# Kernel optimization log

Measured on AMD Instinct MI355X. Metric: run time of the kernel, lower is better.

The kernel has to match this reference:

```python
import jax, jax.numpy as jnp
import numpy as np

HEADS, DIM_HEAD, WINDOW, QK_SCALE = 8, 64, 512, 8.0

def layer_norm(x, g, b, eps=1e-5):
    m = jnp.mean(x, axis=-1, keepdims=True)
    v = jnp.mean(jnp.square(x - m), axis=-1, keepdims=True)
    return (x - m) * jax.lax.rsqrt(v + eps) * g + b

def l2norm(x, eps=1e-12):
    n = jnp.linalg.norm(x, axis=-1, keepdims=True)
    return x / jnp.maximum(n, eps)

def rotate_half(x):
    x1, x2 = jnp.split(x, 2, axis=-1)
    return jnp.concatenate([-x2, x1], axis=-1)

def rotary_xpos(n, dim, scale_base):
    # SinusoidalEmbeddings with use_xpos=True, scale_base = window_size // 2
    inv_freq = 1.0 / (10000.0 ** (jnp.arange(0, dim, 2, dtype=jnp.float32) / dim))
    t = jnp.arange(n, dtype=jnp.float32)
    freqs = t[:, None] * inv_freq[None, :]
    freqs = jnp.concatenate([freqs, freqs], axis=-1)  # (n, dim)
    scale_vec = (jnp.arange(0, dim, 2, dtype=jnp.float32) + 0.4 * dim) / (1.4 * dim)
    power = (t - n // 2) / scale_base
    scale = scale_vec[None, :] ** power[:, None]
    scale = jnp.concatenate([scale, scale], axis=-1)  # (n, dim)
    return freqs, scale

def local_attention(q, k, v):
    # q, k, v: (BH, N, D); causal sliding-window attention, look_backward=1, exact windowsize
    BH, N, D = q.shape
    WS = WINDOW
    W = N // WS
    freqs, xscale = rotary_xpos(N, D, WS // 2)
    cos, sin = jnp.cos(freqs), jnp.sin(freqs)
    q = q * cos * xscale + rotate_half(q) * sin * xscale
    k = k * cos / xscale + rotate_half(k) * sin / xscale

    bq = q.reshape(BH, W, WS, D)
    bk = k.reshape(BH, W, WS, D)
    bv = v.reshape(BH, W, WS, D)

    def look_around(x):  # prepend previous window along key axis -> (BH, W, 2*WS, D)
        padded = jnp.pad(x, ((0, 0), (1, 0), (0, 0), (0, 0)))
        return jnp.concatenate([padded[:, :-1], padded[:, 1:]], axis=2)

    bk2, bv2 = look_around(bk), look_around(bv)

    seq = jnp.arange(N)
    bq_t = seq.reshape(W, WS)
    kpos = jnp.pad(seq.reshape(W, WS), ((1, 0), (0, 0)), constant_values=-1)
    bq_k = jnp.concatenate([kpos[:-1], kpos[1:]], axis=1)  # (W, 2*WS)
    i, j = bq_t[:, :, None], bq_k[:, None, :]
    # causal | exact-windowsize | padding
    mask = (i < j) | (i > j + WS) | (j == -1)

    sim = jnp.einsum('bwid,bwjd->bwij', bq, bk2) * QK_SCALE
    sim = jnp.where(mask[None], -jnp.finfo(sim.dtype).max, sim)
    attn = jax.nn.softmax(sim, axis=-1)
    out = jnp.einsum('bwij,bwjd->bwid', attn, bv2)
    return out.reshape(BH, N, D)

def reference(x, attn_ln_g, attn_ln_b, Wqkv, q_scale, k_scale, Wout,
              ff_ln_g, ff_ln_b, ff_W1, ff_b1, ff_W2, ff_b2):
    B, N, D = x.shape
    H, DH = HEADS, DIM_HEAD
    # --- LocalMHA (prenorm, qk_rmsnorm, rotary xpos, causal window) ---
    h = layer_norm(x, attn_ln_g, attn_ln_b)
    qkv = (h @ Wqkv).reshape(B, N, 3, H, DH)
    q = jnp.moveaxis(qkv[:, :, 0], 2, 1)  # (B, H, N, DH)
    k = jnp.moveaxis(qkv[:, :, 1], 2, 1)
    v = jnp.moveaxis(qkv[:, :, 2], 2, 1)
    q = l2norm(q) * q_scale
    k = l2norm(k) * k_scale
    q = q.reshape(B * H, N, DH)
    k = k.reshape(B * H, N, DH)
    v = v.reshape(B * H, N, DH)
    o = local_attention(q, k, v).reshape(B, H, N, DH)
    o = jnp.moveaxis(o, 1, 2).reshape(B, N, H * DH) @ Wout
    x = x + o
    # --- FeedForward: LN -> Linear -> GEGLU -> Linear ---
    h = layer_norm(x, ff_ln_g, ff_ln_b)
    u = h @ ff_W1 + ff_b1
    a, gate = jnp.split(u, 2, axis=-1)
    x = x + ((a * jax.nn.gelu(gate, approximate=False)) @ ff_W2 + ff_b2)
    return x

def setup_inputs():
    key = jax.random.key(0)
    ks = jax.random.split(key, 6)
    B, N, D = 2, 8192, 512
    H, DH = HEADS, DIM_HEAD
    HID = int(D * 4 * 2 / 3)  # 1365
    s = 0.02
    return {
        'x': jax.random.normal(ks[0], (B, N, D), jnp.float32),
        'attn_ln_g': jnp.ones((D,), jnp.float32),
        'attn_ln_b': jnp.zeros((D,), jnp.float32),
        'Wqkv': jax.random.normal(ks[1], (D, 3 * H * DH), jnp.float32) * s,
        'q_scale': jnp.ones((DH,), jnp.float32),
        'k_scale': jnp.ones((DH,), jnp.float32),
        'Wout': jax.random.normal(ks[2], (H * DH, D), jnp.float32) * s,
        'ff_ln_g': jnp.ones((D,), jnp.float32),
        'ff_ln_b': jnp.zeros((D,), jnp.float32),
        'ff_W1': jax.random.normal(ks[3], (D, 2 * HID), jnp.float32) * s,
        'ff_b1': jnp.zeros((2 * HID,), jnp.float32),
        'ff_W2': jax.random.normal(ks[4], (HID, D), jnp.float32) * s,
        'ff_b2': jnp.zeros((D,), jnp.float32),
    }
```

## Files before the change

kernel.cpp:

```cpp
#include <hip/hip_runtime.h>
#include <cstdint>
#include <cstddef>

typedef __bf16 bf16;
typedef __bf16 bf16x8 __attribute__((ext_vector_type(8)));
typedef float  f32x4  __attribute__((ext_vector_type(4)));

#define MFMA16(a, b, c) __builtin_amdgcn_mfma_f32_16x16x32_bf16((a), (b), (c), 0, 0, 0)

static __device__ __forceinline__ void gld16(const bf16* g, bf16* l) {
    __builtin_amdgcn_global_load_lds(
        (const __attribute__((address_space(1))) void*)g,
        (__attribute__((address_space(3))) void*)l, 16, 0, 0);
}

static __device__ __forceinline__ unsigned pack_bf16x2(bf16 a, bf16 b) {
    union { unsigned u; bf16 h[2]; } t;
    t.h[0] = a; t.h[1] = b;
    return t.u;
}

static __device__ __forceinline__ void tcvt_block(const float* __restrict__ src,
                                                  bf16* __restrict__ dst,
                                                  int K, int N, int Kpad, int Nrows,
                                                  int bkx, int bny, int tid,
                                                  float (*t)[33]) {
    int tx = tid & 31, ty = tid >> 5;
    int k0 = bkx * 32, n0 = bny * 32;
#pragma unroll
    for (int i = ty; i < 32; i += 8) {
        int k = k0 + i, n = n0 + tx;
        t[i][tx] = (k < K && n < N) ? src[(size_t)k * N + n] : 0.f;
    }
    __syncthreads();
#pragma unroll
    for (int i = ty; i < 32; i += 8) {
        int n = n0 + i, k = k0 + tx;
        if (n < Nrows && k < Kpad) dst[(size_t)n * Kpad + k] = (bf16)t[tx][i];
    }
}

__global__ __launch_bounds__(256) void prep_kernel(
    const float* __restrict__ x, const float* __restrict__ g,
    const float* __restrict__ b, bf16* __restrict__ h,
    const float* __restrict__ Wqkv, bf16* __restrict__ WqkvT,
    const float* __restrict__ Wout, bf16* __restrict__ WoutT,
    const float* __restrict__ W1, bf16* __restrict__ W1T,
    const float* __restrict__ W2, bf16* __restrict__ W2T) {
    __shared__ float t[32][33];
    const int bid = blockIdx.x;
    const int tid = threadIdx.x;
    if (bid < 4096) {
        int row  = bid * 4 + (tid >> 6);
        int lane = tid & 63;
        const float* xr = x + (size_t)row * 512 + lane * 8;
        float4 v0 = *(const float4*)xr;
        float4 v1 = *(const float4*)(xr + 4);
        float s  = v0.x + v0.y + v0.z + v0.w + v1.x + v1.y + v1.z + v1.w;
        float ss = v0.x*v0.x + v0.y*v0.y + v0.z*v0.z + v0.w*v0.w
                 + v1.x*v1.x + v1.y*v1.y + v1.z*v1.z + v1.w*v1.w;
#pragma unroll
        for (int off = 1; off < 64; off <<= 1) {
            s  += __shfl_xor(s, off, 64);
            ss += __shfl_xor(ss, off, 64);
        }
        float mean = s * (1.0f / 512.0f);
        float var  = ss * (1.0f / 512.0f) - mean * mean;
        float rstd = rsqrtf(var + 1e-5f);
        const float* gr = g + lane * 8;
        const float* br = b + lane * 8;
        float4 g0 = *(const float4*)gr, g1 = *(const float4*)(gr + 4);
        float4 b0 = *(const float4*)br, b1 = *(const float4*)(br + 4);
        bf16x8 o;
        o[0] = (bf16)((v0.x - mean) * rstd * g0.x + b0.x);
        o[1] = (bf16)((v0.y - mean) * rstd * g0.y + b0.y);
        o[2] = (bf16)((v0.z - mean) * rstd * g0.z + b0.z);
        o[3] = (bf16)((v0.w - mean) * rstd * g0.w + b0.w);
        o[4] = (bf16)((v1.x - mean) * rstd * g1.x + b1.x);
        o[5] = (bf16)((v1.y - mean) * rstd * g1.y + b1.y);
        o[6] = (bf16)((v1.z - mean) * rstd * g1.z + b1.z);
        o[7] = (bf16)((v1.w - mean) * rstd * g1.w + b1.w);
        *(uint4*)(h + (size_t)row * 512 + lane * 8) = *(uint4*)&o;
    } else if (bid < 4096 + 768) {
        int bb = bid - 4096;
        tcvt_block(Wqkv, WqkvT, 512, 1536, 512, 1536, bb & 15, bb >> 4, tid, t);
    } else if (bid < 4096 + 768 + 256) {
        int bb = bid - (4096 + 768);
        tcvt_block(Wout, WoutT, 512, 512, 512, 512, bb & 15, bb >> 4, tid, t);
    } else if (bid < 4096 + 768 + 256 + 1408) {
        int bb = bid - (4096 + 768 + 256);
        tcvt_block(W1, W1T, 512, 2730, 512, 2816, bb & 15, bb >> 4, tid, t);
    } else {
        int bb = bid - (4096 + 768 + 256 + 1408);
        tcvt_block(W2, W2T, 1365, 512, 1408, 512, bb % 44, bb / 44, tid, t);
    }
}

__global__ __launch_bounds__(256) void ln_kernel(const float* __restrict__ x,
                                                 const float* __restrict__ g,
                                                 const float* __restrict__ b,
                                                 bf16* __restrict__ out) {
    int row  = blockIdx.x * 4 + (threadIdx.x >> 6);
    int lane = threadIdx.x & 63;
    const float* xr = x + (size_t)row * 512 + lane * 8;
    float4 v0 = *(const float4*)xr;
    float4 v1 = *(const float4*)(xr + 4);
    float s  = v0.x + v0.y + v0.z + v0.w + v1.x + v1.y + v1.z + v1.w;
    float ss = v0.x*v0.x + v0.y*v0.y + v0.z*v0.z + v0.w*v0.w
             + v1.x*v1.x + v1.y*v1.y + v1.z*v1.z + v1.w*v1.w;
#pragma unroll
    for (int off = 1; off < 64; off <<= 1) {
        s  += __shfl_xor(s, off, 64);
        ss += __shfl_xor(ss, off, 64);
    }
    float mean = s * (1.0f / 512.0f);
    float var  = ss * (1.0f / 512.0f) - mean * mean;
    float rstd = rsqrtf(var + 1e-5f);
    const float* gr = g + lane * 8;
    const float* br = b + lane * 8;
    float4 g0 = *(const float4*)gr, g1 = *(const float4*)(gr + 4);
    float4 b0 = *(const float4*)br, b1 = *(const float4*)(br + 4);
    bf16x8 o;
    o[0] = (bf16)((v0.x - mean) * rstd * g0.x + b0.x);
    o[1] = (bf16)((v0.y - mean) * rstd * g0.y + b0.y);
    o[2] = (bf16)((v0.z - mean) * rstd * g0.z + b0.z);
    o[3] = (bf16)((v0.w - mean) * rstd * g0.w + b0.w);
    o[4] = (bf16)((v1.x - mean) * rstd * g1.x + b1.x);
    o[5] = (bf16)((v1.y - mean) * rstd * g1.y + b1.y);
    o[6] = (bf16)((v1.z - mean) * rstd * g1.z + b1.z);
    o[7] = (bf16)((v1.w - mean) * rstd * g1.w + b1.w);
    *(uint4*)(out + (size_t)row * 512 + lane * 8) = *(uint4*)&o;
}

template <int EPI>
__global__ __launch_bounds__(256, (EPI == 0 ? 3 : 4)) void gemm_bt(
    const bf16* __restrict__ A, const bf16* __restrict__ Bm, int K,
    bf16* __restrict__ Cb, float* Cf,
    const float* res, const float* __restrict__ bias) {
    __shared__ __align__(16) bf16 As[128 * 64];
    __shared__ __align__(16) bf16 Bs[128 * 64];
    const int tid  = threadIdx.x;
    const int wid  = tid >> 6;
    const int lane = tid & 63;
    const int quad = lane >> 4;
    const int l16  = lane & 15;
    const int wm   = wid >> 1;
    const int wn   = wid & 1;
    const int m0   = blockIdx.y * 128;
    const int n0   = blockIdx.x * 128;

    f32x4 z4 = {0.f, 0.f, 0.f, 0.f};
    f32x4 acc[4][4];
#pragma unroll
    for (int i = 0; i < 4; ++i)
#pragma unroll
        for (int j = 0; j < 4; ++j) acc[i][j] = z4;

    for (int kt = 0; kt < K; kt += 64) {
        __syncthreads();
#pragma unroll
        for (int p = 0; p < 4; ++p) {
            int c   = tid + (p << 8);
            int row = c >> 3;
            int g   = (c & 7) ^ (row & 7);
            gld16(A  + (size_t)(m0 + row) * K + kt + g * 8, As + c * 8);
            gld16(Bm + (size_t)(n0 + row) * K + kt + g * 8, Bs + c * 8);
        }
        __syncthreads();
#pragma unroll
        for (int ks = 0; ks < 2; ++ks) {
            bf16x8 af[4], bfr[4];
#pragma unroll
            for (int i = 0; i < 4; ++i) {
                int r = wm * 64 + i * 16 + l16;
                af[i] = *(const bf16x8*)(As + r * 64 + ((((ks << 2) + quad)) ^ (r & 7)) * 8);
            }
#pragma unroll
            for (int j = 0; j < 4; ++j) {
                int r = wn * 64 + j * 16 + l16;
                bfr[j] = *(const bf16x8*)(Bs + r * 64 + ((((ks << 2) + quad)) ^ (r & 7)) * 8);
            }
#pragma unroll
            for (int i = 0; i < 4; ++i)
#pragma unroll
                for (int j = 0; j < 4; ++j)
                    acc[i][j] = MFMA16(af[i], bfr[j], acc[i][j]);
        }
    }

    if (EPI == 0) {
        const int nbase = n0 + wn * 64;
        const int which = nbase >> 9;
        const int hh    = (nbase >> 6) & 7;
        if (which == 2) {
#pragma unroll
            for (int i = 0; i < 4; ++i)
#pragma unroll
                for (int j = 0; j < 4; ++j)
#pragma unroll
                    for (int r = 0; r < 4; ++r) {
                        int m = m0 + wm * 64 + i * 16 + quad * 4 + r;
                        int d = j * 16 + l16;
                        int bb = m >> 13, nn = m & 8191;
                        Cb[(size_t)2 * 8388608 +
                           ((size_t)(bb * 8 + hh) * 8192 + nn) * 64 + d] =
                            (bf16)acc[i][j][r];
                    }
        } else {
            const float* scale = (which == 0) ? res : bias;
            const float sgn = (which == 0) ? 1.0f : -1.0f;
            float sc[4], revf[4], lg[4];
#pragma unroll
            for (int j = 0; j < 4; ++j) {
                int d  = j * 16 + l16;
                int i2 = d & 31;
                sc[j]   = scale[d];
                revf[j] = __builtin_exp2f(-(float)i2 * 0.4152410118609190f) *
                          0.15915494309189535f;
                lg[j]   = __builtin_log2f(((float)(2 * i2) + 25.6f) * (1.0f / 89.6f));
            }
            const size_t obase = (size_t)which * 8388608;
#pragma unroll
            for (int i = 0; i < 4; ++i)
#pragma unroll
                for (int r = 0; r < 4; ++r) {
                    int m = m0 + wm * 64 + i * 16 + quad * 4 + r;
                    int bb = m >> 13, nn = m & 8191;
                    float ss = 0.f;
#pragma unroll
                    for (int j = 0; j < 4; ++j) ss += acc[i][j][r] * acc[i][j][r];
                    ss += __shfl_xor(ss, 1, 64);
                    ss += __shfl_xor(ss, 2, 64);
                    ss += __shfl_xor(ss, 4, 64);
                    ss += __shfl_xor(ss, 8, 64);
                    float rn = rsqrtf(fmaxf(ss, 1e-24f));
                    float val[4];
#pragma unroll
                    for (int j = 0; j < 4; ++j) val[j] = acc[i][j][r] * rn * sc[j];
                    float fn = (float)nn;
                    float pw = (fn - 4096.0f) * (1.0f / 256.0f) * sgn;
#pragma unroll
                    for (int j = 0; j < 4; ++j) {
                        float xrev = fn * revf[j];
                        xrev -= floorf(xrev);
                        float cv = __builtin_amdgcn_cosf(xrev);
                        float sv = __builtin_amdgcn_sinf(xrev);
                        float xs = __builtin_exp2f(pw * lg[j]);
                        float rh = (j < 2) ? -val[j ^ 2] : val[j ^ 2];
                        float ov = (val[j] * cv + rh * sv) * xs;
                        int d = j * 16 + l16;
                        Cb[obase + ((size_t)(bb * 8 + hh) * 8192 + nn) * 64 + d] =
                            (bf16)ov;
                    }
                }
        }
    } else {
#pragma unroll
        for (int i = 0; i < 4; ++i)
#pragma unroll
            for (int j = 0; j < 4; ++j)
#pragma unroll
                for (int r = 0; r < 4; ++r) {
                    int m = m0 + wm * 64 + i * 16 + quad * 4 + r;
                    int n = n0 + wn * 64 + j * 16 + l16;
                    float v = acc[i][j][r];
                    size_t idx = (size_t)m * 512 + n;
                    if (EPI == 1) {
                        Cf[idx] = v + res[idx];
                    } else {
                        float rv = res[idx];
                        Cf[idx] = v + rv + bias[n];
                    }
                }
    }
}

__global__ __launch_bounds__(256) void attn_kernel(const bf16* __restrict__ q,
                                                   const bf16* __restrict__ k,
                                                   const bf16* __restrict__ v,
                                                   bf16* __restrict__ o) {
    __shared__ __align__(16) bf16 Ks[128 * 64];
    __shared__ __align__(16) bf16 Vt[64][136];
    __shared__ __align__(16) bf16 Ps[4][16][136];
    const int tid  = threadIdx.x;
    const int wid  = tid >> 6;
    const int lane = tid & 63;
    const int quad = lane >> 4;
    const int l16  = lane & 15;
    const int lid = (blockIdx.x & 7) * 128 + (blockIdx.x >> 3);
    const int bh  = lid >> 6;
    const int q0  = (lid & 63) * 128;
    const size_t base = (size_t)bh * 8192;

    bf16x8 aq[2][2];
#pragma unroll
    for (int mt = 0; mt < 2; ++mt) {
        int qrow = q0 + wid * 32 + mt * 16 + l16;
        const bf16* qp = q + (base + qrow) * 64 + quad * 8;
        aq[mt][0] = *(const bf16x8*)qp;
        aq[mt][1] = *(const bf16x8*)(qp + 32);
    }
    f32x4 z4 = {0.f, 0.f, 0.f, 0.f};
    f32x4 accO[2][4];
    float rs[2][4];
#pragma unroll
    for (int mt = 0; mt < 2; ++mt)
#pragma unroll
        for (int j = 0; j < 4; ++j) { accO[mt][j] = z4; rs[mt][j] = 0.f; }

    int klo = q0 - 512;
    if (klo < 0) klo = 0;
    for (int kc = klo; kc < q0 + 128; kc += 128) {
        __syncthreads();
#pragma unroll
        for (int p = 0; p < 4; ++p) {
            int c   = tid + (p << 8);
            int row = c >> 3;
            int g   = (c & 7) ^ (row & 7);
            gld16(k + (base + kc + row) * 64 + g * 8, Ks + c * 8);
        }
        {
            int kp = lane;
#pragma unroll
            for (int w2 = 0; w2 < 2; ++w2) {
                int dc = wid * 2 + w2;
                const bf16* vp = v + (base + kc + kp * 2) * 64 + dc * 8;
                union { uint4 u; bf16 h[8]; } va, vb2;
                va.u  = *(const uint4*)vp;
                vb2.u = *(const uint4*)(vp + 64);
#pragma unroll
                for (int j = 0; j < 8; ++j)
                    *(unsigned*)&Vt[dc * 8 + j][kp * 2] =
                        pack_bf16x2(va.h[j], vb2.h[j]);
            }
        }
        __syncthreads();
#pragma unroll
        for (int mt = 0; mt < 2; ++mt) {
            f32x4 s[8];
#pragma unroll
            for (int ns = 0; ns < 8; ++ns) {
                int row = ns * 16 + l16;
                bf16x8 b0 = *(const bf16x8*)(Ks + row * 64 + ((quad    ) ^ (row & 7)) * 8);
                bf16x8 b1 = *(const bf16x8*)(Ks + row * 64 + ((4 + quad) ^ (row & 7)) * 8);
                f32x4 t = z4;
                t = MFMA16(aq[mt][0], b0, t);
                t = MFMA16(aq[mt][1], b1, t);
                s[ns] = t;
            }
            int gi0 = q0 + wid * 32 + mt * 16 + quad * 4;
#pragma unroll
            for (int ns = 0; ns < 8; ++ns) {
                int gj = kc + ns * 16 + l16;
#pragma unroll
                for (int r = 0; r < 4; ++r) {
                    int e = gi0 + r - gj;
                    float p = __builtin_exp2f(
                        fmaf(s[ns][r], 11.541560327f, -11.541560327f));
                    p = ((unsigned)e <= 512u) ? p : 0.f;
                    rs[mt][r] += p;
                    Ps[wid][quad * 4 + r][ns * 16 + l16] = (bf16)p;
                }
            }
#pragma unroll
            for (int ks2 = 0; ks2 < 4; ++ks2) {
                bf16x8 ap = *(const bf16x8*)&Ps[wid][l16][ks2 * 32 + quad * 8];
#pragma unroll
                for (int ds = 0; ds < 4; ++ds) {
                    bf16x8 bv = *(const bf16x8*)&Vt[ds * 16 + l16][ks2 * 32 + quad * 8];
                    accO[mt][ds] = MFMA16(ap, bv, accO[mt][ds]);
                }
            }
        }
    }
#pragma unroll
    for (int mt = 0; mt < 2; ++mt)
#pragma unroll
        for (int r = 0; r < 4; ++r) {
            float t = rs[mt][r];
            t += __shfl_xor(t, 1, 64);
            t += __shfl_xor(t, 2, 64);
            t += __shfl_xor(t, 4, 64);
            t += __shfl_xor(t, 8, 64);
            rs[mt][r] = 1.0f / t;
        }
    int bb = bh >> 3, hh = bh & 7;
#pragma unroll
    for (int mt = 0; mt < 2; ++mt)
#pragma unroll
        for (int ds = 0; ds < 4; ++ds)
#pragma unroll
            for (int r = 0; r < 4; ++r) {
                int m = q0 + wid * 32 + mt * 16 + quad * 4 + r;
                o[((size_t)(bb * 8192 + m)) * 512 + hh * 64 + ds * 16 + l16] =
                    (bf16)(accO[mt][ds][r] * rs[mt][r]);
            }
}

__global__ __launch_bounds__(256, 4) void ff1_kernel(const bf16* __restrict__ A,
                                                     const bf16* __restrict__ W1T,
                                                     const float* __restrict__ b1,
                                                     bf16* __restrict__ act) {
    __shared__ __align__(16) bf16 As[128 * 64];
    __shared__ __align__(16) bf16 Bsa[64 * 64];
    __shared__ __align__(16) bf16 Bsg[64 * 64];
    const int tid  = threadIdx.x;
    const int wid  = tid >> 6;
    const int lane = tid & 63;
    const int quad = lane >> 4;
    const int l16  = lane & 15;
    const int wm   = wid >> 1;
    const int wn   = wid & 1;
    const int m0   = blockIdx.y * 128;
    const int n0   = blockIdx.x * 64;

    f32x4 z4 = {0.f, 0.f, 0.f, 0.f};
    f32x4 aa[4][2], ag[4][2];
#pragma unroll
    for (int i = 0; i < 4; ++i)
#pragma unroll
        for (int j = 0; j < 2; ++j) { aa[i][j] = z4; ag[i][j] = z4; }

    for (int kt = 0; kt < 512; kt += 64) {
        __syncthreads();
#pragma unroll
        for (int p = 0; p < 4; ++p) {
            int c   = tid + (p << 8);
            int row = c >> 3;
            int g   = (c & 7) ^ (row & 7);
            gld16(A + (size_t)(m0 + row) * 512 + kt + g * 8, As + c * 8);
        }
#pragma unroll
        for (int p = 0; p < 2; ++p) {
            int c   = tid + (p << 8);
            int row = c >> 3;
            int g   = (c & 7) ^ (row & 7);
            gld16(W1T + (size_t)(n0 + row) * 512 + kt + g * 8, Bsa + c * 8);
            gld16(W1T + (size_t)(1365 + n0 + row) * 512 + kt + g * 8, Bsg + c * 8);
        }
        __syncthreads();
#pragma unroll
        for (int ks = 0; ks < 2; ++ks) {
            bf16x8 af[4];
#pragma unroll
            for (int i = 0; i < 4; ++i) {
                int r = wm * 64 + i * 16 + l16;
                af[i] = *(const bf16x8*)(As + r * 64 + ((((ks << 2) + quad)) ^ (r & 7)) * 8);
            }
#pragma unroll
            for (int j = 0; j < 2; ++j) {
                int r = wn * 32 + j * 16 + l16;
                int sl = (((ks << 2) + quad)) ^ (r & 7);
                bf16x8 ba = *(const bf16x8*)(Bsa + r * 64 + sl * 8);
                bf16x8 bg = *(const bf16x8*)(Bsg + r * 64 + sl * 8);
#pragma unroll
                for (int i = 0; i < 4; ++i) {
                    aa[i][j] = MFMA16(af[i], ba, aa[i][j]);
                    ag[i][j] = MFMA16(af[i], bg, ag[i][j]);
                }
            }
        }
    }

#pragma unroll
    for (int i = 0; i < 4; ++i)
#pragma unroll
        for (int j = 0; j < 2; ++j)
#pragma unroll
            for (int r = 0; r < 4; ++r) {
                int m  = m0 + wm * 64 + i * 16 + quad * 4 + r;
                int n  = n0 + wn * 32 + j * 16 + l16;
                bf16 outv = (bf16)0.f;
                if (n < 1365) {
                    float av = aa[i][j][r] + b1[n];
                    float gv = ag[i][j][r] + b1[1365 + n];
                    float gel = 0.5f * gv * (1.0f + erff(gv * 0.70710678118f));
                    outv = (bf16)(av * gel);
                }
                act[(size_t)m * 1408 + n] = outv;
            }
}

extern "C" void kernel_launch(void* const* d_in, const int* in_sizes, int n_in,
                              void* d_out, int out_size, void* d_ws, size_t ws_size,
                              hipStream_t stream) {
    const float* x      = (const float*)d_in[0];
    const float* ln1g   = (const float*)d_in[1];
    const float* ln1b   = (const float*)d_in[2];
    const float* Wqkv   = (const float*)d_in[3];
    const float* qscale = (const float*)d_in[4];
    const float* kscale = (const float*)d_in[5];
    const float* Wout   = (const float*)d_in[6];
    const float* ln2g   = (const float*)d_in[7];
    const float* ln2b   = (const float*)d_in[8];
    const float* W1     = (const float*)d_in[9];
    const float* b1     = (const float*)d_in[10];
    const float* W2     = (const float*)d_in[11];
    const float* b2     = (const float*)d_in[12];
    float* out = (float*)d_out;

    char* ws = (char*)d_ws;
    const size_t MB = 1024 * 1024;
    bf16* h   = (bf16*)(ws);
    bf16* qb  = (bf16*)(ws + 16 * MB);
    bf16* kb  = (bf16*)(ws + 32 * MB);
    bf16* vb  = (bf16*)(ws + 48 * MB);
    bf16* wts = (bf16*)(ws + 64 * MB);
    bf16* WqkvT = wts;
    bf16* WoutT = WqkvT + 1536 * 512;
    bf16* W1T   = WoutT + 512 * 512;
    bf16* W2T   = W1T + 2816 * 512;
    bf16* ob  = h;
    bf16* h2  = h;
    bf16* act = qb;
    float* x1 = out;

    prep_kernel<<<4096 + 768 + 256 + 1408 + 704, 256, 0, stream>>>(
        x, ln1g, ln1b, h, Wqkv, WqkvT, Wout, WoutT, W1, W1T, W2, W2T);
    gemm_bt<0><<<dim3(12, 128), 256, 0, stream>>>(h, WqkvT, 512, qb, nullptr,
                                                  qscale, kscale);
    attn_kernel<<<1024, 256, 0, stream>>>(qb, kb, vb, ob);
    gemm_bt<1><<<dim3(4, 128), 256, 0, stream>>>(ob, WoutT, 512, nullptr, x1, x, nullptr);
    ln_kernel<<<4096, 256, 0, stream>>>(x1, ln2g, ln2b, h2);
    ff1_kernel<<<dim3(22, 128), 256, 0, stream>>>(h2, W1T, b1, act);
    gemm_bt<2><<<dim3(4, 128), 256, 0, stream>>>(act, W2T, 1408, nullptr, out, x1, b2);
}
```

Measured before the change: 350.4 us.

## Shrink attention key tile to 64, transpose QK MFMA for packed P stores

The attention kernel now processes keys in 64-row chunks instead of 128, which shrinks shared memory for K, V^T and P and adds a launch-bounds occupancy hint of 4 blocks. The QK^T MFMA operands are swapped so each lane holds a contiguous run of 4 keys for one query. That lets P be written to LDS as one packed 8-byte store instead of scattered 2-byte stores, and lets the row-sum reduction use fewer shuffles. The trade-off is twice as many loop iterations and __syncthreads barriers per block, plus extra per-row shuffles in the epilogue to redistribute the normalisers.

Measured after the change: 346.1 us. No clear change (-1.2%).

```diff
diff --git a/kernel.cpp b/kernel.cpp
--- a/kernel.cpp
+++ b/kernel.cpp
@@ -275,13 +275,13 @@
     }
 }
 
-__global__ __launch_bounds__(256) void attn_kernel(const bf16* __restrict__ q,
-                                                   const bf16* __restrict__ k,
-                                                   const bf16* __restrict__ v,
-                                                   bf16* __restrict__ o) {
-    __shared__ __align__(16) bf16 Ks[128 * 64];
-    __shared__ __align__(16) bf16 Vt[64][136];
-    __shared__ __align__(16) bf16 Ps[4][16][136];
+__global__ __launch_bounds__(256, 4) void attn_kernel(const bf16* __restrict__ q,
+                                                      const bf16* __restrict__ k,
+                                                      const bf16* __restrict__ v,
+                                                      bf16* __restrict__ o) {
+    __shared__ __align__(16) bf16 Ks[64 * 64];
+    __shared__ __align__(16) bf16 Vt[64][72];
+    __shared__ __align__(16) bf16 Ps[4][16][72];
     const int tid  = threadIdx.x;
     const int wid  = tid >> 6;
     const int lane = tid & 63;
@@ -291,6 +291,7 @@
     const int bh  = lid >> 6;
     const int q0  = (lid & 63) * 128;
     const size_t base = (size_t)bh * 8192;
+    const float CE = 11.541560327f;
 
     bf16x8 aq[2][2];
 #pragma unroll
@@ -302,68 +303,65 @@
     }
     f32x4 z4 = {0.f, 0.f, 0.f, 0.f};
     f32x4 accO[2][4];
-    float rs[2][4];
+    float rs[2] = {0.f, 0.f};
 #pragma unroll
     for (int mt = 0; mt < 2; ++mt)
 #pragma unroll
-        for (int j = 0; j < 4; ++j) { accO[mt][j] = z4; rs[mt][j] = 0.f; }
+        for (int j = 0; j < 4; ++j) accO[mt][j] = z4;
 
     int klo = q0 - 512;
     if (klo < 0) klo = 0;
-    for (int kc = klo; kc < q0 + 128; kc += 128) {
+    for (int kc = klo; kc < q0 + 128; kc += 64) {
         __syncthreads();
 #pragma unroll
-        for (int p = 0; p < 4; ++p) {
+        for (int p = 0; p < 2; ++p) {
             int c   = tid + (p << 8);
             int row = c >> 3;
             int g   = (c & 7) ^ (row & 7);
             gld16(k + (base + kc + row) * 64 + g * 8, Ks + c * 8);
         }
         {
-            int kp = lane;
-#pragma unroll
-            for (int w2 = 0; w2 < 2; ++w2) {
-                int dc = wid * 2 + w2;
-                const bf16* vp = v + (base + kc + kp * 2) * 64 + dc * 8;
-                union { uint4 u; bf16 h[8]; } va, vb2;
-                va.u  = *(const uint4*)vp;
-                vb2.u = *(const uint4*)(vp + 64);
-#pragma unroll
-                for (int j = 0; j < 8; ++j)
-                    *(unsigned*)&Vt[dc * 8 + j][kp * 2] =
-                        pack_bf16x2(va.h[j], vb2.h[j]);
-            }
+            int dc = tid >> 5, kp = tid & 31;
+            const bf16* vp = v + (base + kc + kp * 2) * 64 + dc * 8;
+            union { uint4 u; bf16 h[8]; } va, vb2;
+            va.u  = *(const uint4*)vp;
+            vb2.u = *(const uint4*)(vp + 64);
+#pragma unroll
+            for (int j = 0; j < 8; ++j)
+                *(unsigned*)&Vt[dc * 8 + j][kp * 2] = pack_bf16x2(va.h[j], vb2.h[j]);
         }
         __syncthreads();
 #pragma unroll
         for (int mt = 0; mt < 2; ++mt) {
-            f32x4 s[8];
-#pragma unroll
-            for (int ns = 0; ns < 8; ++ns) {
+            const int qrow = q0 + wid * 32 + mt * 16 + l16;
+            f32x4 s[4];
+#pragma unroll
+            for (int ns = 0; ns < 4; ++ns) {
                 int row = ns * 16 + l16;
-                bf16x8 b0 = *(const bf16x8*)(Ks + row * 64 + ((quad    ) ^ (row & 7)) * 8);
-                bf16x8 b1 = *(const bf16x8*)(Ks + row * 64 + ((4 + quad) ^ (row & 7)) * 8);
+                bf16x8 kf0 = *(const bf16x8*)(Ks + row * 64 + ((quad    ) ^ (row & 7)) * 8);
+                bf16x8 kf1 = *(const bf16x8*)(Ks + row * 64 + ((4 + quad) ^ (row & 7)) * 8);
                 f32x4 t = z4;
-                t = MFMA16(aq[mt][0], b0, t);
-                t = MFMA16(aq[mt][1], b1, t);
+                t = MFMA16(kf0, aq[mt][0], t);
+                t = MFMA16(kf1, aq[mt][1], t);
                 s[ns] = t;
             }
-            int gi0 = q0 + wid * 32 + mt * 16 + quad * 4;
-#pragma unroll
-            for (int ns = 0; ns < 8; ++ns) {
-                int gj = kc + ns * 16 + l16;
+#pragma unroll
+            for (int ns = 0; ns < 4; ++ns) {
+                int e0 = qrow - (kc + ns * 16 + quad * 4);
+                float p[4];
 #pragma unroll
                 for (int r = 0; r < 4; ++r) {
-                    int e = gi0 + r - gj;
-                    float p = __builtin_exp2f(
-                        fmaf(s[ns][r], 11.541560327f, -11.541560327f));
-                    p = ((unsigned)e <= 512u) ? p : 0.f;
-                    rs[mt][r] += p;
-                    Ps[wid][quad * 4 + r][ns * 16 + l16] = (bf16)p;
+                    float pv = __builtin_exp2f(fmaf(s[ns][r], CE, -CE));
+                    p[r] = ((unsigned)(e0 - r) <= 512u) ? pv : 0.f;
                 }
-            }
-#pragma unroll
-            for (int ks2 = 0; ks2 < 4; ++ks2) {
+                rs[mt] += (p[0] + p[1]) + (p[2] + p[3]);
+                union { uint2 v2; unsigned w[2]; } pk;
+                pk.w[0] = pack_bf16x2((bf16)p[0], (bf16)p[1]);
+                pk.w[1] = pack_bf16x2((bf16)p[2], (bf16)p[3]);
+                *(uint2*)&Ps[wid][l16][ns * 16 + quad * 4] = pk.v2;
+            }
+#pragma unroll
+            for (int ks2 = 0; ks2 < 2; ++ks2) {
                 bf16x8 ap = *(const bf16x8*)&Ps[wid][l16][ks2 * 32 + quad * 8];
 #pragma unroll
                 for (int ds = 0; ds < 4; ++ds) {
@@ -374,27 +372,24 @@
         }
     }
 #pragma unroll
+    for (int mt = 0; mt < 2; ++mt) {
+        float t = rs[mt];
+        t += __shfl_xor(t, 16, 64);
+        t += __shfl_xor(t, 32, 64);
+        rs[mt] = 1.0f / t;
+    }
+    int bb = bh >> 3, hh = bh & 7;
+#pragma unroll
     for (int mt = 0; mt < 2; ++mt)
 #pragma unroll
         for (int r = 0; r < 4; ++r) {
-            float t = rs[mt][r];
-            t += __shfl_xor(t, 1, 64);
-            t += __shfl_xor(t, 2, 64);
-            t += __shfl_xor(t, 4, 64);
-            t += __shfl_xor(t, 8, 64);
-            rs[mt][r] = 1.0f / t;
-        }
-    int bb = bh >> 3, hh = bh & 7;
-#pragma unroll
-    for (int mt = 0; mt < 2; ++mt)
-#pragma unroll
-        for (int ds = 0; ds < 4; ++ds)
-#pragma unroll
-            for (int r = 0; r < 4; ++r) {
-                int m = q0 + wid * 32 + mt * 16 + quad * 4 + r;
+            float inv = __shfl(rs[mt], quad * 4 + r, 64);
+            int m = q0 + wid * 32 + mt * 16 + quad * 4 + r;
+#pragma unroll
+            for (int ds = 0; ds < 4; ++ds)
                 o[((size_t)(bb * 8192 + m)) * 512 + hh * 64 + ds * 16 + l16] =
-                    (bf16)(accO[mt][ds][r] * rs[mt][r]);
-            }
+                    (bf16)(accO[mt][ds][r] * inv);
+        }
 }
 
 __global__ __launch_bounds__(256, 4) void ff1_kernel(const bf16* __restrict__ A,
```
